# Performance work log

Hardware: AMD Instinct MI355X
Metric: run time of the kernel (lower is better)

## Reference

```python
import jax, jax.numpy as jnp
import numpy as np
import math

E = 1024
H = 16
R = 16
ALPHA = 16
SCALING = ALPHA / R
T, B, S = 2048, 2, 2048


def setup_inputs() -> dict:
    key = jax.random.key(0)
    ks = jax.random.split(key, 20)
    d = {
        "query": jax.random.normal(ks[0], (T, B, E), jnp.float32),
        "key": jax.random.normal(ks[1], (S, B, E), jnp.float32),
        "value": jax.random.normal(ks[2], (S, B, E), jnp.float32),
    }
    i = 3
    for name in ("q", "k", "v", "o"):
        d[name + "_w"] = jax.random.normal(ks[i], (E, E), jnp.float32) * 0.02; i += 1
        d[name + "_b"] = jax.random.normal(ks[i], (E,), jnp.float32) * 0.02; i += 1
        d[name + "_la"] = jax.random.normal(ks[i], (R, E), jnp.float32) * 0.02; i += 1
        d[name + "_lb"] = jax.random.normal(ks[i], (E, R), jnp.float32) * 0.02; i += 1
    return d


def _lora_linear(x, w, b, la, lb):
    # y = x @ w.T + b + scaling * (x @ la.T) @ lb.T
    return x @ w.T + b + SCALING * ((x @ la.T) @ lb.T)


def reference(query, key, value,
              q_w, q_b, q_la, q_lb,
              k_w, k_b, k_la, k_lb,
              v_w, v_b, v_la, v_lb,
              o_w, o_b, o_la, o_lb):
    tgt_len, bsz, embed_dim = query.shape
    src_len = key.shape[0]
    head_dim = embed_dim // H
    q = _lora_linear(query, q_w, q_b, q_la, q_lb)
    k = _lora_linear(key, k_w, k_b, k_la, k_lb)
    v = _lora_linear(value, v_w, v_b, v_la, v_lb)
    # (T, B, E) -> (B*H, T, hd)
    q = q.reshape(tgt_len, bsz * H, head_dim).transpose(1, 0, 2)
    k = k.reshape(src_len, bsz * H, head_dim).transpose(1, 0, 2)
    v = v.reshape(src_len, bsz * H, head_dim).transpose(1, 0, 2)
    scale = 1.0 / math.sqrt(float(head_dim))
    scores = jnp.einsum("btd,bsd->bts", q * scale, k)  # (B*H, T, S)
    attn = jax.nn.softmax(scores, axis=-1)
    out = jnp.einsum("bts,bsd->btd", attn, v)  # (B*H, T, hd)
    out = out.transpose(1, 0, 2).reshape(tgt_len * bsz, embed_dim)
    out = _lora_linear(out, o_w, o_b, o_la, o_lb)
    out = out.reshape(tgt_len, bsz, embed_dim)
    attn_w = attn.reshape(bsz, H, tgt_len, src_len).mean(axis=1)
    return out, attn_w
```

## Files before the change

kernel.cpp:

```cpp
#include <hip/hip_runtime.h>
#include <stdint.h>

#define E_DIM 1024
#define KAUG 1056
#define N_HEADS 16
#define HD 64
#define R_LORA 16
#define T_LEN 2048
#define B_SZ 2
#define S_LEN 2048
#define NROW 4096
#define Q_SCALE 0.1803368801111204f

#define XG_N ((size_t)NROW * KAUG)
#define WG_N ((size_t)E_DIM * KAUG)
#define HSZ  ((size_t)B_SZ * N_HEADS * T_LEN * HD)

typedef unsigned short USH;
typedef __bf16 bf16x8 __attribute__((ext_vector_type(8)));
typedef float  f32x4  __attribute__((ext_vector_type(4)));

__device__ __forceinline__ USH f2bf(float f) {
    uint32_t u = __builtin_bit_cast(uint32_t, f);
    return (USH)((u + 0x7FFFu + ((u >> 16) & 1u)) >> 16);
}
__device__ __forceinline__ float bf2f(USH s) {
    uint32_t u = ((uint32_t)s) << 16;
    return __builtin_bit_cast(float, u);
}
__device__ __forceinline__ void async_cp16(const void* g, void* l) {
    __builtin_amdgcn_global_load_lds(
        (const __attribute__((address_space(1))) void*)g,
        (__attribute__((address_space(3))) void*)l, 16, 0, 0);
}
__device__ __forceinline__ uint32_t pack_bf_trunc(float x, float y) {
    return __builtin_amdgcn_perm(__builtin_bit_cast(uint32_t, y),
                                 __builtin_bit_cast(uint32_t, x), 0x07060302u);
}

__global__ __launch_bounds__(256) void lora_aug_x3_kernel(
    const float* __restrict__ Xq, const float* __restrict__ Xk,
    const float* __restrict__ Xv,
    const float* __restrict__ laq, const float* __restrict__ lak,
    const float* __restrict__ lav, USH* __restrict__ Xg_base) {
    int n = blockIdx.x, y = blockIdx.y, tid = threadIdx.x;
    const float* X  = (y == 0) ? Xq : (y == 1) ? Xk : Xv;
    const float* la = (y == 0) ? laq : (y == 1) ? lak : lav;
    USH* Xg = Xg_base + (size_t)y * XG_N;

    float4 xv = *(const float4*)(X + (size_t)n * E_DIM + tid * 4);
    ushort4 ox;
    ox.x = f2bf(xv.x); ox.y = f2bf(xv.y); ox.z = f2bf(xv.z); ox.w = f2bf(xv.w);
    *(ushort4*)(Xg + (size_t)n * KAUG + tid * 4) = ox;

    float acc[R_LORA];
#pragma unroll
    for (int r = 0; r < R_LORA; ++r) {
        float4 lv = *(const float4*)(la + (size_t)r * E_DIM + tid * 4);
        acc[r] = xv.x * lv.x + xv.y * lv.y + xv.z * lv.z + xv.w * lv.w;
    }
#pragma unroll
    for (int r = 0; r < R_LORA; ++r) {
        float v = acc[r];
#pragma unroll
        for (int off = 32; off > 0; off >>= 1) v += __shfl_down(v, off, 64);
        acc[r] = v;
    }
    __shared__ float red[R_LORA][4];
    int lane = tid & 63, wid = tid >> 6;
    if (lane == 0) {
#pragma unroll
        for (int r = 0; r < R_LORA; ++r) red[r][wid] = acc[r];
    }
    __syncthreads();
    if (tid < 32) {
        float v = 0.0f;
        if (tid < R_LORA) v = red[tid][0] + red[tid][1] + red[tid][2] + red[tid][3];
        else if (tid == R_LORA) v = 1.0f;
        Xg[(size_t)n * KAUG + 1024 + tid] = f2bf(v);
    }
}

__global__ __launch_bounds__(256) void lora_a_bf16_kernel(
    USH* __restrict__ Xg, const float* __restrict__ la) {
    int n = blockIdx.x, tid = threadIdx.x;
    ushort4 xu = *(const ushort4*)(Xg + (size_t)n * KAUG + tid * 4);
    float x0 = bf2f(xu.x), x1 = bf2f(xu.y), x2 = bf2f(xu.z), x3 = bf2f(xu.w);
    float acc[R_LORA];
#pragma unroll
    for (int r = 0; r < R_LORA; ++r) {
        float4 lv = *(const float4*)(la + (size_t)r * E_DIM + tid * 4);
        acc[r] = x0 * lv.x + x1 * lv.y + x2 * lv.z + x3 * lv.w;
    }
#pragma unroll
    for (int r = 0; r < R_LORA; ++r) {
        float v = acc[r];
#pragma unroll
        for (int off = 32; off > 0; off >>= 1) v += __shfl_down(v, off, 64);
        acc[r] = v;
    }
    __shared__ float red[R_LORA][4];
    int lane = tid & 63, wid = tid >> 6;
    if (lane == 0) {
#pragma unroll
        for (int r = 0; r < R_LORA; ++r) red[r][wid] = acc[r];
    }
    __syncthreads();
    if (tid < 32) {
        float v = 0.0f;
        if (tid < R_LORA) v = red[tid][0] + red[tid][1] + red[tid][2] + red[tid][3];
        else if (tid == R_LORA) v = 1.0f;
        Xg[(size_t)n * KAUG + 1024 + tid] = f2bf(v);
    }
}

__global__ __launch_bounds__(256) void aug_w4_kernel(
    const float* __restrict__ Wq, const float* __restrict__ lbq, const float* __restrict__ bq,
    const float* __restrict__ Wk, const float* __restrict__ lbk, const float* __restrict__ bk_,
    const float* __restrict__ Wv, const float* __restrict__ lbv, const float* __restrict__ bv_,
    const float* __restrict__ Wo, const float* __restrict__ lbo, const float* __restrict__ bo,
    USH* __restrict__ Wg_base) {
    int e = blockIdx.x, y = blockIdx.y, tid = threadIdx.x;
    const float* W    = (y == 0) ? Wq : (y == 1) ? Wk : (y == 2) ? Wv : Wo;
    const float* lb   = (y == 0) ? lbq : (y == 1) ? lbk : (y == 2) ? lbv : lbo;
    const float* bias = (y == 0) ? bq : (y == 1) ? bk_ : (y == 2) ? bv_ : bo;
    USH* Wg = Wg_base + (size_t)y * WG_N;

    float4 v = *(const float4*)(W + (size_t)e * E_DIM + tid * 4);
    ushort4 o;
    o.x = f2bf(v.x); o.y = f2bf(v.y); o.z = f2bf(v.z); o.w = f2bf(v.w);
    *(ushort4*)(Wg + (size_t)e * KAUG + tid * 4) = o;
    if (tid < 32) {
        float t = (tid < R_LORA) ? lb[(size_t)e * R_LORA + tid]
                                 : (tid == R_LORA ? bias[e] : 0.0f);
        Wg[(size_t)e * KAUG + 1024 + tid] = f2bf(t);
    }
}

__global__ __launch_bounds__(256) void gemm_qkv_kernel(
    const USH* __restrict__ Xg_base, const USH* __restrict__ Wg_base,
    USH* __restrict__ qkv_base) {
    __shared__ __align__(16) USH As[128 * 32];
    __shared__ __align__(16) USH Bs[128 * 32];

    int orig = blockIdx.x + (blockIdx.y << 3) + blockIdx.z * 256;
    int v_ = (orig & 7) * 96 + (orig >> 3);
    int e0 = (v_ & 7) * 128, n0 = ((v_ >> 3) & 31) * 128, z = v_ >> 8;

    const USH* Xg = Xg_base + (size_t)z * XG_N;
    const USH* Wg = Wg_base + (size_t)z * WG_N;
    USH* out = qkv_base + (size_t)z * HSZ;
    float scale = (z == 0) ? Q_SCALE : 1.0f;

    int tid = threadIdx.x;
    int wid = tid >> 6, lane = tid & 63, quad = lane >> 4, l16 = lane & 15;
    int wm = wid & 1, wn = wid >> 1;

    int r0 = wid * 16 + (lane >> 2);
    int k8 = (lane & 3) * 8;

    f32x4 acc[4][4];
    const f32x4 fzero = {0.f, 0.f, 0.f, 0.f};
#pragma unroll
    for (int i = 0; i < 4; ++i)
#pragma unroll
        for (int j = 0; j < 4; ++j) acc[i][j] = fzero;

    for (int kt = 0; kt < KAUG; kt += 32) {
        __syncthreads();
        async_cp16(Xg + (size_t)(n0 + r0) * KAUG + kt + k8,       As + (wid * 16) * 32);
        async_cp16(Xg + (size_t)(n0 + 64 + r0) * KAUG + kt + k8,  As + (64 + wid * 16) * 32);
        async_cp16(Wg + (size_t)(e0 + r0) * KAUG + kt + k8,       Bs + (wid * 16) * 32);
        async_cp16(Wg + (size_t)(e0 + 64 + r0) * KAUG + kt + k8,  Bs + (64 + wid * 16) * 32);
        __syncthreads();

        bf16x8 af[4], bfr[4];
#pragma unroll
        for (int i = 0; i < 4; ++i)
            af[i] = *(const bf16x8*)&As[(wm * 64 + i * 16 + l16) * 32 + quad * 8];
#pragma unroll
        for (int j = 0; j < 4; ++j)
            bfr[j] = *(const bf16x8*)&Bs[(wn * 64 + j * 16 + l16) * 32 + quad * 8];
#pragma unroll
        for (int i = 0; i < 4; ++i)
#pragma unroll
            for (int j = 0; j < 4; ++j)
                acc[i][j] = __builtin_amdgcn_mfma_f32_16x16x32_bf16(
                    af[i], bfr[j], acc[i][j], 0, 0, 0);
    }

#pragma unroll
    for (int i = 0; i < 4; ++i) {
#pragma unroll
        for (int j = 0; j < 4; ++j) {
#pragma unroll
            for (int r = 0; r < 4; ++r) {
                int nr = n0 + wm * 64 + i * 16 + quad * 4 + r;
                int ec = e0 + wn * 64 + j * 16 + l16;
                float v = acc[i][j][r] * scale;
                int b = nr & 1, h = ec >> 6, d = ec & 63;
                if (z != 2) {
                    int t = nr >> 1;
                    out[(((size_t)(b * 16 + h) * T_LEN + t) << 6) + d] = f2bf(v);
                } else {
                    int s = nr >> 1;
                    out[(((size_t)(b * 16 + h) * HD + d) << 11) + s] = f2bf(v);
                }
            }
        }
    }
}

__device__ __forceinline__ void gemm_mainloop(
    const USH* __restrict__ Xg, const USH* __restrict__ Wg,
    USH* As, USH* Bs, int n0, int e0, f32x4 (&acc)[2][4]) {
    int tid = threadIdx.x;
    int wid = tid >> 6, lane = tid & 63, quad = lane >> 4, l16 = lane & 15;
    int wm = wid & 1, wn = wid >> 1;
    int r0 = wid * 16 + (lane >> 2);
    int k8 = (lane & 3) * 8;

    for (int kt = 0; kt < KAUG; kt += 32) {
        __syncthreads();
        async_cp16(Xg + (size_t)(n0 + r0) * KAUG + kt + k8,       As + (wid * 16) * 32);
        async_cp16(Wg + (size_t)(e0 + r0) * KAUG + kt + k8,       Bs + (wid * 16) * 32);
        async_cp16(Wg + (size_t)(e0 + 64 + r0) * KAUG + kt + k8,  Bs + (64 + wid * 16) * 32);
        __syncthreads();

        bf16x8 af[2], bfr[4];
#pragma unroll
        for (int i = 0; i < 2; ++i)
            af[i] = *(const bf16x8*)&As[(wm * 32 + i * 16 + l16) * 32 + quad * 8];
#pragma unroll
        for (int j = 0; j < 4; ++j)
            bfr[j] = *(const bf16x8*)&Bs[(wn * 64 + j * 16 + l16) * 32 + quad * 8];
#pragma unroll
        for (int i = 0; i < 2; ++i)
#pragma unroll
            for (int j = 0; j < 4; ++j)
                acc[i][j] = __builtin_amdgcn_mfma_f32_16x16x32_bf16(
                    af[i], bfr[j], acc[i][j], 0, 0, 0);
    }
}

__global__ __launch_bounds__(256) void gemm_o_kernel(
    const USH* __restrict__ Xg, const USH* __restrict__ Wg,
    float* __restrict__ out) {
    __shared__ __align__(16) USH As[64 * 32];
    __shared__ __align__(16) USH Bs[128 * 32];

    int orig = blockIdx.x + (blockIdx.y << 3);
    int v_ = ((orig & 7) << 6) + (orig >> 3);
    int e0 = (v_ & 7) * 128, n0 = (v_ >> 3) * 64;

    int tid = threadIdx.x;
    int wid = tid >> 6, lane = tid & 63, quad = lane >> 4, l16 = lane & 15;
    int wm = wid & 1, wn = wid >> 1;

    f32x4 acc[2][4];
    const f32x4 fzero = {0.f, 0.f, 0.f, 0.f};
#pragma unroll
    for (int i = 0; i < 2; ++i)
#pragma unroll
        for (int j = 0; j < 4; ++j) acc[i][j] = fzero;

    gemm_mainloop(Xg, Wg, As, Bs, n0, e0, acc);

#pragma unroll
    for (int i = 0; i < 2; ++i)
#pragma unroll
        for (int j = 0; j < 4; ++j)
#pragma unroll
            for (int r = 0; r < 4; ++r) {
                int nr = n0 + wm * 32 + i * 16 + quad * 4 + r;
                int ec = e0 + wn * 64 + j * 16 + l16;
                out[(size_t)nr * E_DIM + ec] = acc[i][j][r];
            }
}

__global__ __launch_bounds__(256, 2) void flash_mfma_kernel(
    const USH* __restrict__ qp, const USH* __restrict__ kp,
    const USH* __restrict__ vpt, USH* __restrict__ ohg,
    float* __restrict__ lbuf) {
    __shared__ __align__(16) USH QPs[8192];
    __shared__ __align__(16) USH Ks[2][4096];
    __shared__ __align__(16) USH Vs[2][4096];

    int orig = blockIdx.x + (blockIdx.y << 4);
    int v_ = ((orig & 7) << 6) + (orig >> 3);
    int t0 = (v_ & 15) * 128, bh = v_ >> 4;

    int tid = threadIdx.x, w = tid >> 6, lane = tid & 63;
    int quad = lane >> 4, l16 = lane & 15;
    int sw = l16 & 7;
    size_t headO = (size_t)bh * (T_LEN * HD);

#pragma unroll
    for (int ii = 0; ii < 2; ++ii) {
        int i = w * 2 + ii;
#pragma unroll
        for (int half = 0; half < 2; ++half)
            async_cp16(qp + headO + (size_t)(t0 + i * 16 + l16) * HD + half * 32 + quad * 8,
                       QPs + i * 1024 + half * 512);
    }
#pragma unroll
    for (int half = 0; half < 2; ++half) {
        async_cp16(kp + headO + (size_t)(w * 16 + l16) * HD + half * 32 + quad * 8,
                   &Ks[0][w * 1024 + half * 512]);
        async_cp16(vpt + headO + (size_t)(w * 16 + l16) * S_LEN + half * 32 + quad * 8,
                   &Vs[0][w * 1024 + half * 512]);
    }
    __syncthreads();

    bf16x8 bq[2][2];
#pragma unroll
    for (int i2 = 0; i2 < 2; ++i2)
#pragma unroll
        for (int half = 0; half < 2; ++half)
            bq[i2][half] = *(const bf16x8*)&QPs[(w * 2 + i2) * 1024 + half * 512 + quad * 128 + l16 * 8];

    float lsum[2] = {0.f, 0.f};
    const f32x4 fzero = {0.f, 0.f, 0.f, 0.f};
    f32x4 o[2][4];
#pragma unroll
    for (int i2 = 0; i2 < 2; ++i2)
#pragma unroll
        for (int jd = 0; jd < 4; ++jd) o[i2][jd] = fzero;

    for (int s0 = 0; s0 < S_LEN; s0 += 64) {
        int cur = (s0 >> 6) & 1;
        if (s0 + 64 < S_LEN) {
#pragma unroll
            for (int half = 0; half < 2; ++half) {
                async_cp16(kp + headO + (size_t)(s0 + 64 + w * 16 + l16) * HD + half * 32 + quad * 8,
                           &Ks[cur ^ 1][w * 1024 + half * 512]);
                async_cp16(vpt + headO + (size_t)(w * 16 + l16) * S_LEN + s0 + 64 + half * 32 + quad * 8,
                           &Vs[cur ^ 1][w * 1024 + half * 512]);
            }
        }

        bf16x8 ak[4][2];
#pragma unroll
        for (int j = 0; j < 4; ++j)
#pragma unroll
            for (int half = 0; half < 2; ++half)
                ak[j][half] = *(const bf16x8*)&Ks[cur][j * 1024 + half * 512 + quad * 128 + l16 * 8];

#pragma unroll
        for (int i2 = 0; i2 < 2; ++i2) {
            f32x4 sc[4];
#pragma unroll
            for (int j = 0; j < 4; ++j) {
                sc[j] = __builtin_amdgcn_mfma_f32_16x16x32_bf16(ak[j][0], bq[i2][0], fzero, 0, 0, 0);
                sc[j] = __builtin_amdgcn_mfma_f32_16x16x32_bf16(ak[j][1], bq[i2][1], sc[j], 0, 0, 0);
            }
            float ls = 0.f;
#pragma unroll
            for (int j = 0; j < 4; ++j)
#pragma unroll
                for (int r = 0; r < 4; ++r) {
                    float p = exp2f(sc[j][r]);
                    sc[j][r] = p;
                    ls += p;
                }
            lsum[i2] += ls;
            USH* pb = QPs + w * 2048 + i2 * 1024;
#pragma unroll
            for (int j = 0; j < 4; ++j) {
                uint2 dv;
                dv.x = pack_bf_trunc(sc[j][0], sc[j][1]);
                dv.y = pack_bf_trunc(sc[j][2], sc[j][3]);
                int g = (j * 2 + (quad >> 1)) ^ sw;
                *(uint2*)&pb[l16 * 64 + g * 8 + (quad & 1) * 4] = dv;
            }
        }

        bf16x8 bv[4][2];
#pragma unroll
        for (int jd = 0; jd < 4; ++jd)
#pragma unroll
            for (int half = 0; half < 2; ++half)
                bv[jd][half] = *(const bf16x8*)&Vs[cur][jd * 1024 + half * 512 + quad * 128 + l16 * 8];

#pragma unroll
        for (int i2 = 0; i2 < 2; ++i2) {
            const USH* pb = QPs + w * 2048 + i2 * 1024;
            bf16x8 ap0 = *(const bf16x8*)&pb[l16 * 64 + (quad ^ sw) * 8];
            bf16x8 ap1 = *(const bf16x8*)&pb[l16 * 64 + ((4 + quad) ^ sw) * 8];
#pragma unroll
            for (int jd = 0; jd < 4; ++jd) {
                o[i2][jd] = __builtin_amdgcn_mfma_f32_16x16x32_bf16(ap0, bv[jd][0], o[i2][jd], 0, 0, 0);
                o[i2][jd] = __builtin_amdgcn_mfma_f32_16x16x32_bf16(ap1, bv[jd][1], o[i2][jd], 0, 0, 0);
            }
        }

        __syncthreads();
    }

#pragma unroll
    for (int i2 = 0; i2 < 2; ++i2) {
        lsum[i2] += __shfl_xor(lsum[i2], 16, 64);
        lsum[i2] += __shfl_xor(lsum[i2], 32, 64);
    }

    int b = bh >> 4, h = bh & 15;
#pragma unroll
    for (int i2 = 0; i2 < 2; ++i2) {
        float inv[4];
#pragma unroll
        for (int r = 0; r < 4; ++r)
            inv[r] = 1.0f / __shfl(lsum[i2], (lane & 48) | (quad * 4 + r), 64);
#pragma unroll
        for (int jd = 0; jd < 4; ++jd)
#pragma unroll
            for (int r = 0; r < 4; ++r) {
                int t = t0 + w * 32 + i2 * 16 + quad * 4 + r;
                int n = t * 2 + b, e = h * 64 + jd * 16 + l16;
                ohg[(size_t)n * KAUG + e] = f2bf(o[i2][jd][r] * inv[r]);
            }
        if (quad == 0)
            lbuf[(size_t)bh * T_LEN + t0 + w * 32 + i2 * 16 + l16] = lsum[i2];
    }
}

__global__ __launch_bounds__(256, 4) void attnw_mfma_kernel(
    const USH* __restrict__ qp, const USH* __restrict__ kp,
    const float* __restrict__ lbuf, float* __restrict__ aw) {
    __shared__ __align__(16) USH Ks[2][4096];

    int orig = blockIdx.x + (blockIdx.y << 5) + (blockIdx.z << 9);
    int v_ = ((orig & 7) << 7) + (orig >> 3);
    int s0 = (v_ & 31) * 64, t0 = ((v_ >> 5) & 15) * 128, b = v_ >> 9;

    int tid = threadIdx.x, w = tid >> 6, lane = tid & 63;
    int quad = lane >> 4, l16 = lane & 15;

    const f32x4 fzero = {0.f, 0.f, 0.f, 0.f};
    f32x4 acc[2][4];
#pragma unroll
    for (int i2 = 0; i2 < 2; ++i2)
#pragma unroll
        for (int j = 0; j < 4; ++j) acc[i2][j] = fzero;

    {
        size_t head0 = (size_t)(b * 16) * (T_LEN * HD);
#pragma unroll
        for (int half = 0; half < 2; ++half)
            async_cp16(kp + head0 + (size_t)(s0 + w * 16 + l16) * HD + half * 32 + quad * 8,
                       &Ks[0][w * 1024 + half * 512]);
    }
    __syncthreads();

    for (int h = 0; h < N_HEADS; ++h) {
        int bh = b * 16 + h;
        size_t head = (size_t)bh * (T_LEN * HD);
        int cur = h & 1;

        if (h + 1 < N_HEADS) {
            size_t headn = head + (size_t)(T_LEN * HD);
#pragma unroll
            for (int half = 0; half < 2; ++half)
                async_cp16(kp + headn + (size_t)(s0 + w * 16 + l16) * HD + half * 32 + quad * 8,
                           &Ks[cur ^ 1][w * 1024 + half * 512]);
        }

        bf16x8 aq[2][2];
#pragma unroll
        for (int i2 = 0; i2 < 2; ++i2) {
            int i = w * 2 + i2;
            const USH* qrow = qp + head + (size_t)(t0 + i * 16 + l16) * HD + quad * 8;
            aq[i2][0] = *(const bf16x8*)qrow;
            aq[i2][1] = *(const bf16x8*)(qrow + 32);
        }

        float il[2][4];
#pragma unroll
        for (int i2 = 0; i2 < 2; ++i2)
#pragma unroll
            for (int r = 0; r < 4; ++r) {
                int t = t0 + w * 32 + i2 * 16 + quad * 4 + r;
                il[i2][r] = 1.0f / lbuf[(size_t)bh * T_LEN + t];
            }

        bf16x8 bk[4][2];
#pragma unroll
        for (int j = 0; j < 4; ++j)
#pragma unroll
            for (int half = 0; half < 2; ++half)
                bk[j][half] = *(const bf16x8*)&Ks[cur][j * 1024 + half * 512 + quad * 128 + l16 * 8];

#pragma unroll
        for (int i2 = 0; i2 < 2; ++i2) {
#pragma unroll
            for (int j = 0; j < 4; ++j) {
                f32x4 s = __builtin_amdgcn_mfma_f32_16x16x32_bf16(aq[i2][0], bk[j][0], fzero, 0, 0, 0);
                s = __builtin_amdgcn_mfma_f32_16x16x32_bf16(aq[i2][1], bk[j][1], s, 0, 0, 0);
#pragma unroll
                for (int r = 0; r < 4; ++r)
                    acc[i2][j][r] += exp2f(s[r]) * il[i2][r];
            }
        }

        __syncthreads();
    }

    const float inv_h = 1.0f / (float)N_HEADS;
#pragma unroll
    for (int i2 = 0; i2 < 2; ++i2)
#pragma unroll
        for (int j = 0; j < 4; ++j)
#pragma unroll
            for (int r = 0; r < 4; ++r) {
                int t = t0 + w * 32 + i2 * 16 + quad * 4 + r;
                aw[(size_t)b * T_LEN * S_LEN + (size_t)t * S_LEN + s0 + j * 16 + l16] =
                    acc[i2][j][r] * inv_h;
            }
}

extern "C" void kernel_launch(void* const* d_in, const int* in_sizes, int n_in,
                              void* d_out, int out_size, void* d_ws, size_t ws_size,
                              hipStream_t stream) {
    (void)in_sizes; (void)n_in; (void)out_size; (void)ws_size;

    const float* query = (const float*)d_in[0];
    const float* key_  = (const float*)d_in[1];
    const float* value = (const float*)d_in[2];
    const float* q_w = (const float*)d_in[3],  *q_b = (const float*)d_in[4];
    const float* q_la = (const float*)d_in[5], *q_lb = (const float*)d_in[6];
    const float* k_w = (const float*)d_in[7],  *k_b = (const float*)d_in[8];
    const float* k_la = (const float*)d_in[9], *k_lb = (const float*)d_in[10];
    const float* v_w = (const float*)d_in[11], *v_b = (const float*)d_in[12];
    const float* v_la = (const float*)d_in[13], *v_lb = (const float*)d_in[14];
    const float* o_w = (const float*)d_in[15], *o_b = (const float*)d_in[16];
    const float* o_la = (const float*)d_in[17], *o_lb = (const float*)d_in[18];

    USH* Xg   = (USH*)d_ws;
    USH* Wg   = Xg + 3 * XG_N;
    USH* qkv  = Wg + 4 * WG_N;
    USH* qp   = qkv;
    USH* kp   = qkv + HSZ;
    USH* vpt  = qkv + 2 * HSZ;
    float* lbuf = (float*)(qkv + 3 * HSZ);

    float* out = (float*)d_out;
    float* aw  = out + (size_t)T_LEN * B_SZ * E_DIM;

    dim3 blk(256);

    lora_aug_x3_kernel<<<dim3(NROW, 3), blk, 0, stream>>>(
        query, key_, value, q_la, k_la, v_la, Xg);
    aug_w4_kernel<<<dim3(E_DIM, 4), blk, 0, stream>>>(
        q_w, q_lb, q_b, k_w, k_lb, k_b, v_w, v_lb, v_b, o_w, o_lb, o_b, Wg);
    gemm_qkv_kernel<<<dim3(E_DIM / 128, NROW / 128, 3), blk, 0, stream>>>(Xg, Wg, qkv);

    flash_mfma_kernel<<<dim3(T_LEN / 128, B_SZ * N_HEADS), blk, 0, stream>>>(
        qp, kp, vpt, Xg, lbuf);
    attnw_mfma_kernel<<<dim3(S_LEN / 64, T_LEN / 128, B_SZ), blk, 0, stream>>>(
        qp, kp, lbuf, aw);

    lora_a_bf16_kernel<<<NROW, blk, 0, stream>>>(Xg, o_la);
    gemm_o_kernel<<<dim3(E_DIM / 128, NROW / 64), blk, 0, stream>>>(
        Xg, Wg + 3 * WG_N, out);
}
```

Measured before the change: 400.3 us.

## Shrink flash tile to 64 query rows, add MFMA priority hints and fast exp2

The flash attention kernel now gives each block 64 query rows (16 per wave) instead of 128. The grid doubles, the Q/P shared buffer halves, and launch bounds allow 4 blocks per CU. This aims for more occupancy and latency hiding, at the cost of reloading K/V tiles twice as often across blocks. MFMA sections are also wrapped in s_setprio, and exp2f is replaced by the hardware exp2 intrinsic in both attention kernels.

Result: no change. 406.7 us (+1.6%).

```diff
diff --git a/kernel.cpp b/kernel.cpp
--- a/kernel.cpp
+++ b/kernel.cpp
@@ -278,17 +278,17 @@
             }
 }
 
-__global__ __launch_bounds__(256, 2) void flash_mfma_kernel(
+__global__ __launch_bounds__(256, 4) void flash_mfma_kernel(
     const USH* __restrict__ qp, const USH* __restrict__ kp,
     const USH* __restrict__ vpt, USH* __restrict__ ohg,
     float* __restrict__ lbuf) {
-    __shared__ __align__(16) USH QPs[8192];
+    __shared__ __align__(16) USH QPs[4096];
     __shared__ __align__(16) USH Ks[2][4096];
     __shared__ __align__(16) USH Vs[2][4096];
 
-    int orig = blockIdx.x + (blockIdx.y << 4);
-    int v_ = ((orig & 7) << 6) + (orig >> 3);
-    int t0 = (v_ & 15) * 128, bh = v_ >> 4;
+    int orig = blockIdx.x + (blockIdx.y << 5);
+    int v_ = ((orig & 7) << 7) + (orig >> 3);
+    int t0 = (v_ & 31) * 64, bh = v_ >> 5;
 
     int tid = threadIdx.x, w = tid >> 6, lane = tid & 63;
     int quad = lane >> 4, l16 = lane & 15;
@@ -296,15 +296,9 @@
     size_t headO = (size_t)bh * (T_LEN * HD);
 
 #pragma unroll
-    for (int ii = 0; ii < 2; ++ii) {
-        int i = w * 2 + ii;
-#pragma unroll
-        for (int half = 0; half < 2; ++half)
-            async_cp16(qp + headO + (size_t)(t0 + i * 16 + l16) * HD + half * 32 + quad * 8,
-                       QPs + i * 1024 + half * 512);
-    }
-#pragma unroll
     for (int half = 0; half < 2; ++half) {
+        async_cp16(qp + headO + (size_t)(t0 + w * 16 + l16) * HD + half * 32 + quad * 8,
+                   QPs + w * 1024 + half * 512);
         async_cp16(kp + headO + (size_t)(w * 16 + l16) * HD + half * 32 + quad * 8,
                    &Ks[0][w * 1024 + half * 512]);
         async_cp16(vpt + headO + (size_t)(w * 16 + l16) * S_LEN + half * 32 + quad * 8,
@@ -312,20 +306,16 @@
     }
     __syncthreads();
 
-    bf16x8 bq[2][2];
-#pragma unroll
-    for (int i2 = 0; i2 < 2; ++i2)
-#pragma unroll
-        for (int half = 0; half < 2; ++half)
-            bq[i2][half] = *(const bf16x8*)&QPs[(w * 2 + i2) * 1024 + half * 512 + quad * 128 + l16 * 8];
-
-    float lsum[2] = {0.f, 0.f};
+    bf16x8 bq[2];
+#pragma unroll
+    for (int half = 0; half < 2; ++half)
+        bq[half] = *(const bf16x8*)&QPs[w * 1024 + half * 512 + quad * 128 + l16 * 8];
+
+    float lsum = 0.f;
     const f32x4 fzero = {0.f, 0.f, 0.f, 0.f};
-    f32x4 o[2][4];
-#pragma unroll
-    for (int i2 = 0; i2 < 2; ++i2)
-#pragma unroll
-        for (int jd = 0; jd < 4; ++jd) o[i2][jd] = fzero;
+    f32x4 o[4];
+#pragma unroll
+    for (int jd = 0; jd < 4; ++jd) o[jd] = fzero;
 
     for (int s0 = 0; s0 < S_LEN; s0 += 64) {
         int cur = (s0 >> 6) & 1;
@@ -346,33 +336,33 @@
             for (int half = 0; half < 2; ++half)
                 ak[j][half] = *(const bf16x8*)&Ks[cur][j * 1024 + half * 512 + quad * 128 + l16 * 8];
 
-#pragma unroll
-        for (int i2 = 0; i2 < 2; ++i2) {
-            f32x4 sc[4];
-#pragma unroll
-            for (int j = 0; j < 4; ++j) {
-                sc[j] = __builtin_amdgcn_mfma_f32_16x16x32_bf16(ak[j][0], bq[i2][0], fzero, 0, 0, 0);
-                sc[j] = __builtin_amdgcn_mfma_f32_16x16x32_bf16(ak[j][1], bq[i2][1], sc[j], 0, 0, 0);
-            }
-            float ls = 0.f;
-#pragma unroll
-            for (int j = 0; j < 4; ++j)
-#pragma unroll
-                for (int r = 0; r < 4; ++r) {
-                    float p = exp2f(sc[j][r]);
-                    sc[j][r] = p;
-                    ls += p;
-                }
-            lsum[i2] += ls;
-            USH* pb = QPs + w * 2048 + i2 * 1024;
-#pragma unroll
-            for (int j = 0; j < 4; ++j) {
-                uint2 dv;
-                dv.x = pack_bf_trunc(sc[j][0], sc[j][1]);
-                dv.y = pack_bf_trunc(sc[j][2], sc[j][3]);
-                int g = (j * 2 + (quad >> 1)) ^ sw;
-                *(uint2*)&pb[l16 * 64 + g * 8 + (quad & 1) * 4] = dv;
-            }
+        f32x4 sc[4];
+        __builtin_amdgcn_s_setprio(1);
+#pragma unroll
+        for (int j = 0; j < 4; ++j) {
+            sc[j] = __builtin_amdgcn_mfma_f32_16x16x32_bf16(ak[j][0], bq[0], fzero, 0, 0, 0);
+            sc[j] = __builtin_amdgcn_mfma_f32_16x16x32_bf16(ak[j][1], bq[1], sc[j], 0, 0, 0);
+        }
+        __builtin_amdgcn_s_setprio(0);
+
+        float ls = 0.f;
+#pragma unroll
+        for (int j = 0; j < 4; ++j)
+#pragma unroll
+            for (int r = 0; r < 4; ++r) {
+                float p = __builtin_amdgcn_exp2f(sc[j][r]);
+                sc[j][r] = p;
+                ls += p;
+            }
+        lsum += ls;
+        USH* pb = QPs + w * 1024;
+#pragma unroll
+        for (int j = 0; j < 4; ++j) {
+            uint2 dv;
+            dv.x = pack_bf_trunc(sc[j][0], sc[j][1]);
+            dv.y = pack_bf_trunc(sc[j][2], sc[j][3]);
+            int g = (j * 2 + (quad >> 1)) ^ sw;
+            *(uint2*)&pb[l16 * 64 + g * 8 + (quad & 1) * 4] = dv;
         }
 
         bf16x8 bv[4][2];
@@ -382,45 +372,37 @@
             for (int half = 0; half < 2; ++half)
                 bv[jd][half] = *(const bf16x8*)&Vs[cur][jd * 1024 + half * 512 + quad * 128 + l16 * 8];
 
-#pragma unroll
-        for (int i2 = 0; i2 < 2; ++i2) {
-            const USH* pb = QPs + w * 2048 + i2 * 1024;
-            bf16x8 ap0 = *(const bf16x8*)&pb[l16 * 64 + (quad ^ sw) * 8];
-            bf16x8 ap1 = *(const bf16x8*)&pb[l16 * 64 + ((4 + quad) ^ sw) * 8];
-#pragma unroll
-            for (int jd = 0; jd < 4; ++jd) {
-                o[i2][jd] = __builtin_amdgcn_mfma_f32_16x16x32_bf16(ap0, bv[jd][0], o[i2][jd], 0, 0, 0);
-                o[i2][jd] = __builtin_amdgcn_mfma_f32_16x16x32_bf16(ap1, bv[jd][1], o[i2][jd], 0, 0, 0);
-            }
-        }
+        bf16x8 ap0 = *(const bf16x8*)&pb[l16 * 64 + (quad ^ sw) * 8];
+        bf16x8 ap1 = *(const bf16x8*)&pb[l16 * 64 + ((4 + quad) ^ sw) * 8];
+        __builtin_amdgcn_s_setprio(1);
+#pragma unroll
+        for (int jd = 0; jd < 4; ++jd) {
+            o[jd] = __builtin_amdgcn_mfma_f32_16x16x32_bf16(ap0, bv[jd][0], o[jd], 0, 0, 0);
+            o[jd] = __builtin_amdgcn_mfma_f32_16x16x32_bf16(ap1, bv[jd][1], o[jd], 0, 0, 0);
+        }
+        __builtin_amdgcn_s_setprio(0);
 
         __syncthreads();
     }
 
-#pragma unroll
-    for (int i2 = 0; i2 < 2; ++i2) {
-        lsum[i2] += __shfl_xor(lsum[i2], 16, 64);
-        lsum[i2] += __shfl_xor(lsum[i2], 32, 64);
-    }
+    lsum += __shfl_xor(lsum, 16, 64);
+    lsum += __shfl_xor(lsum, 32, 64);
 
     int b = bh >> 4, h = bh & 15;
-#pragma unroll
-    for (int i2 = 0; i2 < 2; ++i2) {
-        float inv[4];
-#pragma unroll
-        for (int r = 0; r < 4; ++r)
-            inv[r] = 1.0f / __shfl(lsum[i2], (lane & 48) | (quad * 4 + r), 64);
-#pragma unroll
-        for (int jd = 0; jd < 4; ++jd)
-#pragma unroll
-            for (int r = 0; r < 4; ++r) {
-                int t = t0 + w * 32 + i2 * 16 + quad * 4 + r;
-                int n = t * 2 + b, e = h * 64 + jd * 16 + l16;
-                ohg[(size_t)n * KAUG + e] = f2bf(o[i2][jd][r] * inv[r]);
-            }
-        if (quad == 0)
-            lbuf[(size_t)bh * T_LEN + t0 + w * 32 + i2 * 16 + l16] = lsum[i2];
-    }
+    float inv[4];
+#pragma unroll
+    for (int r = 0; r < 4; ++r)
+        inv[r] = 1.0f / __shfl(lsum, (lane & 48) | (quad * 4 + r), 64);
+#pragma unroll
+    for (int jd = 0; jd < 4; ++jd)
+#pragma unroll
+        for (int r = 0; r < 4; ++r) {
+            int t = t0 + w * 16 + quad * 4 + r;
+            int n = t * 2 + b, e = h * 64 + jd * 16 + l16;
+            ohg[(size_t)n * KAUG + e] = f2bf(o[jd][r] * inv[r]);
+        }
+    if (quad == 0)
+        lbuf[(size_t)bh * T_LEN + t0 + w * 16 + l16] = lsum;
 }
 
 __global__ __launch_bounds__(256, 4) void attnw_mfma_kernel(
@@ -493,11 +475,13 @@
         for (int i2 = 0; i2 < 2; ++i2) {
 #pragma unroll
             for (int j = 0; j < 4; ++j) {
+                __builtin_amdgcn_s_setprio(1);
                 f32x4 s = __builtin_amdgcn_mfma_f32_16x16x32_bf16(aq[i2][0], bk[j][0], fzero, 0, 0, 0);
                 s = __builtin_amdgcn_mfma_f32_16x16x32_bf16(aq[i2][1], bk[j][1], s, 0, 0, 0);
+                __builtin_amdgcn_s_setprio(0);
 #pragma unroll
                 for (int r = 0; r < 4; ++r)
-                    acc[i2][j][r] += exp2f(s[r]) * il[i2][r];
+                    acc[i2][j][r] += __builtin_amdgcn_exp2f(s[r]) * il[i2][r];
             }
         }
 
@@ -553,7 +537,7 @@
         q_w, q_lb, q_b, k_w, k_lb, k_b, v_w, v_lb, v_b, o_w, o_lb, o_b, Wg);
     gemm_qkv_kernel<<<dim3(E_DIM / 128, NROW / 128, 3), blk, 0, stream>>>(Xg, Wg, qkv);
 
-    flash_mfma_kernel<<<dim3(T_LEN / 128, B_SZ * N_HEADS), blk, 0, stream>>>(
+    flash_mfma_kernel<<<dim3(T_LEN / 64, B_SZ * N_HEADS), blk, 0, stream>>>(
         qp, kp, vpt, Xg, lbuf);
     attnw_mfma_kernel<<<dim3(S_LEN / 64, T_LEN / 128, B_SZ), blk, 0, stream>>>(
         qp, kp, lbuf, aw);
```

## Shrink flash blocks to 64 rows, load Q and V directly to registers

Applied to the files above, without the earlier changes.

The flash attention kernel now uses 128-thread blocks covering 64 query rows each, which doubles the grid. Q and V fragments are read straight from global memory into registers, and only K is staged in double-buffered LDS along with a smaller P buffer. The change also wraps the MFMA sections in s_setprio and swaps exp2f for the hardware exp2 builtin in both attention kernels. This cuts LDS use and LDS traffic per block, but the direct V loads are issued in the loop with no prefetch, so their latency may be exposed, and each K tile is now loaded by twice as many blocks.

Result: slower. 418.8 us (+4.6%).

```diff
diff --git a/kernel.cpp b/kernel.cpp
--- a/kernel.cpp
+++ b/kernel.cpp
@@ -278,46 +278,39 @@
             }
 }
 
-__global__ __launch_bounds__(256, 2) void flash_mfma_kernel(
+__global__ __launch_bounds__(128, 2) void flash_mfma_kernel(
     const USH* __restrict__ qp, const USH* __restrict__ kp,
     const USH* __restrict__ vpt, USH* __restrict__ ohg,
     float* __restrict__ lbuf) {
-    __shared__ __align__(16) USH QPs[8192];
     __shared__ __align__(16) USH Ks[2][4096];
-    __shared__ __align__(16) USH Vs[2][4096];
-
-    int orig = blockIdx.x + (blockIdx.y << 4);
-    int v_ = ((orig & 7) << 6) + (orig >> 3);
-    int t0 = (v_ & 15) * 128, bh = v_ >> 4;
+    __shared__ __align__(16) USH Pb[2][2][1024];
+
+    int orig = blockIdx.x + (blockIdx.y << 5);
+    int v_ = ((orig & 7) << 7) + (orig >> 3);
+    int t0 = (v_ & 31) * 64, bh = v_ >> 5;
 
     int tid = threadIdx.x, w = tid >> 6, lane = tid & 63;
     int quad = lane >> 4, l16 = lane & 15;
     int sw = l16 & 7;
     size_t headO = (size_t)bh * (T_LEN * HD);
 
-#pragma unroll
-    for (int ii = 0; ii < 2; ++ii) {
-        int i = w * 2 + ii;
+    bf16x8 bq[2][2];
+#pragma unroll
+    for (int i2 = 0; i2 < 2; ++i2) {
+        const USH* qrow = qp + headO + (size_t)(t0 + w * 32 + i2 * 16 + l16) * HD + quad * 8;
+        bq[i2][0] = *(const bf16x8*)qrow;
+        bq[i2][1] = *(const bf16x8*)(qrow + 32);
+    }
+
+#pragma unroll
+    for (int c = 0; c < 2; ++c) {
+        int jj = w * 2 + c;
 #pragma unroll
         for (int half = 0; half < 2; ++half)
-            async_cp16(qp + headO + (size_t)(t0 + i * 16 + l16) * HD + half * 32 + quad * 8,
-                       QPs + i * 1024 + half * 512);
-    }
-#pragma unroll
-    for (int half = 0; half < 2; ++half) {
-        async_cp16(kp + headO + (size_t)(w * 16 + l16) * HD + half * 32 + quad * 8,
-                   &Ks[0][w * 1024 + half * 512]);
-        async_cp16(vpt + headO + (size_t)(w * 16 + l16) * S_LEN + half * 32 + quad * 8,
-                   &Vs[0][w * 1024 + half * 512]);
+            async_cp16(kp + headO + (size_t)(jj * 16 + l16) * HD + half * 32 + quad * 8,
+                       &Ks[0][jj * 1024 + half * 512]);
     }
     __syncthreads();
-
-    bf16x8 bq[2][2];
-#pragma unroll
-    for (int i2 = 0; i2 < 2; ++i2)
-#pragma unroll
-        for (int half = 0; half < 2; ++half)
-            bq[i2][half] = *(const bf16x8*)&QPs[(w * 2 + i2) * 1024 + half * 512 + quad * 128 + l16 * 8];
 
     float lsum[2] = {0.f, 0.f};
     const f32x4 fzero = {0.f, 0.f, 0.f, 0.f};
@@ -331,12 +324,21 @@
         int cur = (s0 >> 6) & 1;
         if (s0 + 64 < S_LEN) {
 #pragma unroll
-            for (int half = 0; half < 2; ++half) {
-                async_cp16(kp + headO + (size_t)(s0 + 64 + w * 16 + l16) * HD + half * 32 + quad * 8,
-                           &Ks[cur ^ 1][w * 1024 + half * 512]);
-                async_cp16(vpt + headO + (size_t)(w * 16 + l16) * S_LEN + s0 + 64 + half * 32 + quad * 8,
-                           &Vs[cur ^ 1][w * 1024 + half * 512]);
-            }
+            for (int c = 0; c < 2; ++c) {
+                int jj = w * 2 + c;
+#pragma unroll
+                for (int half = 0; half < 2; ++half)
+                    async_cp16(kp + headO + (size_t)(s0 + 64 + jj * 16 + l16) * HD + half * 32 + quad * 8,
+                               &Ks[cur ^ 1][jj * 1024 + half * 512]);
+            }
+        }
+
+        bf16x8 bv[4][2];
+#pragma unroll
+        for (int jd = 0; jd < 4; ++jd) {
+            const USH* vrow = vpt + headO + (size_t)(jd * 16 + l16) * S_LEN + s0 + quad * 8;
+            bv[jd][0] = *(const bf16x8*)vrow;
+            bv[jd][1] = *(const bf16x8*)(vrow + 32);
         }
 
         bf16x8 ak[4][2];
@@ -349,22 +351,24 @@
 #pragma unroll
         for (int i2 = 0; i2 < 2; ++i2) {
             f32x4 sc[4];
+            __builtin_amdgcn_s_setprio(1);
 #pragma unroll
             for (int j = 0; j < 4; ++j) {
                 sc[j] = __builtin_amdgcn_mfma_f32_16x16x32_bf16(ak[j][0], bq[i2][0], fzero, 0, 0, 0);
                 sc[j] = __builtin_amdgcn_mfma_f32_16x16x32_bf16(ak[j][1], bq[i2][1], sc[j], 0, 0, 0);
             }
+            __builtin_amdgcn_s_setprio(0);
             float ls = 0.f;
 #pragma unroll
             for (int j = 0; j < 4; ++j)
 #pragma unroll
                 for (int r = 0; r < 4; ++r) {
-                    float p = exp2f(sc[j][r]);
+                    float p = __builtin_amdgcn_exp2f(sc[j][r]);
                     sc[j][r] = p;
                     ls += p;
                 }
             lsum[i2] += ls;
-            USH* pb = QPs + w * 2048 + i2 * 1024;
+            USH* pb = &Pb[w][i2][0];
 #pragma unroll
             for (int j = 0; j < 4; ++j) {
                 uint2 dv;
@@ -375,23 +379,18 @@
             }
         }
 
-        bf16x8 bv[4][2];
-#pragma unroll
-        for (int jd = 0; jd < 4; ++jd)
-#pragma unroll
-            for (int half = 0; half < 2; ++half)
-                bv[jd][half] = *(const bf16x8*)&Vs[cur][jd * 1024 + half * 512 + quad * 128 + l16 * 8];
-
 #pragma unroll
         for (int i2 = 0; i2 < 2; ++i2) {
-            const USH* pb = QPs + w * 2048 + i2 * 1024;
+            const USH* pb = &Pb[w][i2][0];
             bf16x8 ap0 = *(const bf16x8*)&pb[l16 * 64 + (quad ^ sw) * 8];
             bf16x8 ap1 = *(const bf16x8*)&pb[l16 * 64 + ((4 + quad) ^ sw) * 8];
+            __builtin_amdgcn_s_setprio(1);
 #pragma unroll
             for (int jd = 0; jd < 4; ++jd) {
                 o[i2][jd] = __builtin_amdgcn_mfma_f32_16x16x32_bf16(ap0, bv[jd][0], o[i2][jd], 0, 0, 0);
                 o[i2][jd] = __builtin_amdgcn_mfma_f32_16x16x32_bf16(ap1, bv[jd][1], o[i2][jd], 0, 0, 0);
             }
+            __builtin_amdgcn_s_setprio(0);
         }
 
         __syncthreads();
@@ -497,7 +496,7 @@
                 s = __builtin_amdgcn_mfma_f32_16x16x32_bf16(aq[i2][1], bk[j][1], s, 0, 0, 0);
 #pragma unroll
                 for (int r = 0; r < 4; ++r)
-                    acc[i2][j][r] += exp2f(s[r]) * il[i2][r];
+                    acc[i2][j][r] += __builtin_amdgcn_exp2f(s[r]) * il[i2][r];
             }
         }
 
@@ -553,7 +552,7 @@
         q_w, q_lb, q_b, k_w, k_lb, k_b, v_w, v_lb, v_b, o_w, o_lb, o_b, Wg);
     gemm_qkv_kernel<<<dim3(E_DIM / 128, NROW / 128, 3), blk, 0, stream>>>(Xg, Wg, qkv);
 
-    flash_mfma_kernel<<<dim3(T_LEN / 128, B_SZ * N_HEADS), blk, 0, stream>>>(
+    flash_mfma_kernel<<<dim3(T_LEN / 64, B_SZ * N_HEADS), dim3(128), 0, stream>>>(
         qp, kp, vpt, Xg, lbuf);
     attnw_mfma_kernel<<<dim3(S_LEN / 64, T_LEN / 128, B_SZ), blk, 0, stream>>>(
         qp, kp, lbuf, aw);
```
